# Optimization experiments

Measured on AMD Instinct MI355X. Metric: run time of the kernel, lower is better.

The kernel has to match this reference:

```python
import jax, jax.numpy as jnp
import numpy as np

TEMP = 0.07
N, D = 8192, 256
NUM_CLASSES = 512


def setup_inputs() -> dict:
    key = jax.random.key(0)
    k1, k2 = jax.random.split(key)
    features = jax.random.normal(k1, (N, D), dtype=jnp.float32)
    labels = jax.random.randint(k2, (N,), 0, NUM_CLASSES, dtype=jnp.int64)
    return {"features": features, "labels": labels}


def reference(features, labels):
    n = features.shape[0]
    # L2 normalize rows (torch F.normalize, eps=1e-12)
    norm = jnp.sqrt(jnp.sum(features * features, axis=1, keepdims=True))
    f = features / jnp.maximum(norm, 1e-12)
    # [N, N] cosine similarities scaled by temperature
    logits = jnp.matmul(f, f.T) / TEMP
    # positive-pair mask (same label), excluding self
    mask = (labels[:, None] == labels[None, :]).astype(logits.dtype)
    logits_mask = 1.0 - jnp.eye(n, dtype=logits.dtype)
    mask = mask * logits_mask
    # denominator excludes self-similarity
    exp_logits = jnp.exp(logits) * logits_mask
    log_prob = logits - jnp.log(jnp.sum(exp_logits, axis=1, keepdims=True) + 1e-6)
    mean_log_prob_pos = jnp.sum(mask * log_prob, axis=1) / jnp.clip(jnp.sum(mask, axis=1), 1.0, None)
    return -jnp.mean(mean_log_prob_pos)
```

## Files before the change

### kernel.cpp

```cpp
#include <hip/hip_runtime.h>
#include <hip/hip_bf16.h>

#define N 8192
#define D 256
#define NCLS 512
#define INV_TEMP 14.285714285714286f
#define C1 20.609929155f
#define JSPLIT 16

typedef __bf16 bf16x8 __attribute__((ext_vector_type(8)));
typedef float f32x4 __attribute__((ext_vector_type(4)));

static __device__ __forceinline__ unsigned short f2bf(float x) {
    unsigned int u = __float_as_uint(x);
    u = (u + 0x7fffu + ((u >> 16) & 1u)) >> 16;
    return (unsigned short)u;
}
static __device__ __forceinline__ float bf2f(unsigned short b) {
    return __uint_as_float(((unsigned int)b) << 16);
}

__global__ __launch_bounds__(256) void norm_kernel(const float* __restrict__ feat,
                                                   const int* __restrict__ labels,
                                                   __bf16* __restrict__ fb,
                                                   float* __restrict__ G) {
    const int row = (blockIdx.x * 256 + (int)threadIdx.x) >> 6;
    const int lane = threadIdx.x & 63;
    if (row >= N) return;
    float4 v = reinterpret_cast<const float4*>(feat + (size_t)row * D)[lane];
    float ss = v.x * v.x + v.y * v.y + v.z * v.z + v.w * v.w;
#pragma unroll
    for (int m = 1; m < 64; m <<= 1) ss += __shfl_xor(ss, m);
    const float inv = 1.0f / fmaxf(sqrtf(ss), 1e-12f);
    ushort4 o;
    o.x = f2bf(v.x * inv); o.y = f2bf(v.y * inv);
    o.z = f2bf(v.z * inv); o.w = f2bf(v.w * inv);
    reinterpret_cast<ushort4*>(fb + (size_t)row * D)[lane] = o;
    float* g = G + (size_t)labels[row] * D + lane * 4;
    atomicAdd(&g[0], bf2f(o.x));
    atomicAdd(&g[1], bf2f(o.y));
    atomicAdd(&g[2], bf2f(o.z));
    atomicAdd(&g[3], bf2f(o.w));
}

__global__ __launch_bounds__(256, 4) void supcon_main(const __bf16* __restrict__ fb,
                                                      float* __restrict__ rowD) {
    __shared__ __align__(1024) char lds[32768];
    const int lane = threadIdx.x & 63;
    const int w = threadIdx.x >> 6;
    const int l4 = lane & 15;
    const int lh = lane >> 4;
    const int wrow = blockIdx.x * 128 + w * 32;
    const int jbase = blockIdx.y * (N / JSPLIT);
    const char* fbb = (const char*)fb;

    bf16x8 a[2][8];
#pragma unroll
    for (int mf = 0; mf < 2; ++mf)
#pragma unroll
        for (int k = 0; k < 8; ++k)
            a[mf][k] = *reinterpret_cast<const bf16x8*>(
                fbb + (size_t)(wrow + mf * 16 + l4) * 512 + k * 64 + lh * 16);

    const int s7 = l4 & 7;
    const int lhx = lh ^ (s7 & 3);
    const int b2v = (s7 >> 2) & 1;
    const int rb_common = l4 * 512 + lhx * 16;

    auto stage = [&](int bufsel, int jb) {
#pragma unroll
        for (int r = 0; r < 4; ++r) {
            const int G = r * 256 + (int)threadIdx.x;
            const int row = G >> 5, h = G & 31;
            const char* src = fbb + (size_t)(jb + row) * 512 + ((h ^ (row & 7)) * 16);
            char* dst = lds + bufsel * 16384 + r * 4096 + w * 1024;
            __builtin_amdgcn_global_load_lds(
                (const __attribute__((address_space(1))) void*)src,
                (__attribute__((address_space(3))) void*)dst, 16, 0, 0);
        }
    };

    float dsum[2][4] = {};

    const int njt = (N / JSPLIT) / 32;
    int cur = 0;
    stage(0, jbase);
    __syncthreads();

    for (int jt = 0; jt < njt; ++jt) {
        const int jb = jbase + jt * 32;
        if (jt + 1 < njt) stage(cur ^ 1, jb + 32);

        const char* bb = lds + cur * 16384 + rb_common;
        const char* rb0 = bb + b2v * 64;
        const char* rb1 = bb + 64 - b2v * 64;

        f32x4 c[2][2] = {};
#pragma unroll
        for (int q = 0; q < 4; ++q) {
            bf16x8 b00 = *(const bf16x8*)(rb0 + q * 128);
            bf16x8 b01 = *(const bf16x8*)(rb0 + 8192 + q * 128);
            bf16x8 b10 = *(const bf16x8*)(rb1 + q * 128);
            bf16x8 b11 = *(const bf16x8*)(rb1 + 8192 + q * 128);
            c[0][0] = __builtin_amdgcn_mfma_f32_16x16x32_bf16(a[0][2 * q], b00, c[0][0], 0, 0, 0);
            c[1][0] = __builtin_amdgcn_mfma_f32_16x16x32_bf16(a[1][2 * q], b00, c[1][0], 0, 0, 0);
            c[0][1] = __builtin_amdgcn_mfma_f32_16x16x32_bf16(a[0][2 * q], b01, c[0][1], 0, 0, 0);
            c[1][1] = __builtin_amdgcn_mfma_f32_16x16x32_bf16(a[1][2 * q], b01, c[1][1], 0, 0, 0);
            c[0][0] = __builtin_amdgcn_mfma_f32_16x16x32_bf16(a[0][2 * q + 1], b10, c[0][0], 0, 0, 0);
            c[1][0] = __builtin_amdgcn_mfma_f32_16x16x32_bf16(a[1][2 * q + 1], b10, c[1][0], 0, 0, 0);
            c[0][1] = __builtin_amdgcn_mfma_f32_16x16x32_bf16(a[0][2 * q + 1], b11, c[0][1], 0, 0, 0);
            c[1][1] = __builtin_amdgcn_mfma_f32_16x16x32_bf16(a[1][2 * q + 1], b11, c[1][1], 0, 0, 0);
        }

#pragma unroll
        for (int mf = 0; mf < 2; ++mf) {
#pragma unroll
            for (int cf = 0; cf < 2; ++cf) {
                const f32x4 cc = c[mf][cf];
                if (wrow + mf * 16 == jb + cf * 16) {
#pragma unroll
                    for (int r = 0; r < 4; ++r) {
                        const bool diag = (l4 == lh * 4 + r);
                        dsum[mf][r] += diag ? 0.0f : __builtin_amdgcn_exp2f(cc[r] * C1);
                    }
                } else {
#pragma unroll
                    for (int r = 0; r < 4; ++r)
                        dsum[mf][r] += __builtin_amdgcn_exp2f(cc[r] * C1);
                }
            }
        }
        __syncthreads();
        cur ^= 1;
    }

#pragma unroll
    for (int mf = 0; mf < 2; ++mf) {
#pragma unroll
        for (int r = 0; r < 4; ++r) {
            float v1 = dsum[mf][r];
#pragma unroll
            for (int m = 1; m < 16; m <<= 1) v1 += __shfl_xor(v1, m);
            if (l4 == 0) atomicAdd(&rowD[wrow + mf * 16 + lh * 4 + r], v1);
        }
    }
}

__global__ __launch_bounds__(256) void rowdot_kernel(const __bf16* __restrict__ fb,
                                                     const int* __restrict__ labels,
                                                     const float* __restrict__ G,
                                                     float* __restrict__ rowS) {
    const int row = (blockIdx.x * 256 + (int)threadIdx.x) >> 6;
    const int lane = threadIdx.x & 63;
    if (row >= N) return;
    ushort4 o = reinterpret_cast<const ushort4*>(fb + (size_t)row * D)[lane];
    const float f0 = bf2f(o.x), f1 = bf2f(o.y), f2 = bf2f(o.z), f3 = bf2f(o.w);
    const float4 g = reinterpret_cast<const float4*>(G + (size_t)labels[row] * D)[lane];
    float dot = f0 * g.x + f1 * g.y + f2 * g.z + f3 * g.w;
    float self = f0 * f0 + f1 * f1 + f2 * f2 + f3 * f3;
#pragma unroll
    for (int m = 1; m < 64; m <<= 1) {
        dot += __shfl_xor(dot, m);
        self += __shfl_xor(self, m);
    }
    if (lane == 0) rowS[row] = (dot - self) * INV_TEMP;
}

__global__ __launch_bounds__(256) void finalize_kernel(const int* __restrict__ labels,
                                                       const float* __restrict__ rowD,
                                                       const float* __restrict__ rowS,
                                                       float* __restrict__ out) {
    __shared__ int hist[NCLS];
    __shared__ float red[4];
    for (int i = threadIdx.x; i < NCLS; i += 256) hist[i] = 0;
    __syncthreads();
    for (int i = threadIdx.x; i < N; i += 256) atomicAdd(&hist[labels[i]], 1);
    __syncthreads();
    float local = 0.0f;
    for (int r = threadIdx.x; r < N; r += 256) {
        const float c = (float)(hist[labels[r]] - 1);
        local += (rowS[r] - c * __logf(rowD[r] + 1e-6f)) / fmaxf(c, 1.0f);
    }
#pragma unroll
    for (int m = 1; m < 64; m <<= 1) local += __shfl_xor(local, m);
    if ((threadIdx.x & 63) == 0) red[threadIdx.x >> 6] = local;
    __syncthreads();
    if (threadIdx.x == 0) out[0] = -(red[0] + red[1] + red[2] + red[3]) / (float)N;
}

extern "C" void kernel_launch(void* const* d_in, const int* in_sizes, int n_in,
                              void* d_out, int out_size, void* d_ws, size_t ws_size,
                              hipStream_t stream) {
    const float* feat = (const float*)d_in[0];
    const int* labels = (const int*)d_in[1];

    __bf16* fb = (__bf16*)d_ws;
    float* G = (float*)((char*)d_ws + (size_t)N * D * 2);
    float* rowD = G + (size_t)NCLS * D;
    float* rowS = rowD + N;

    hipMemsetAsync(G, 0, ((size_t)NCLS * D + N) * sizeof(float), stream);
    norm_kernel<<<N / 4, 256, 0, stream>>>(feat, labels, fb, G);
    dim3 grid(N / 128, JSPLIT);
    supcon_main<<<grid, 256, 0, stream>>>(fb, rowD);
    rowdot_kernel<<<N / 4, 256, 0, stream>>>(fb, labels, G, rowS);
    finalize_kernel<<<1, 256, 0, stream>>>(labels, rowD, rowS, (float*)d_out);
}
```

Measured before the change: 143.8 us.

## Enlarge per-wave row tile and replace atomic class sums with ballot gather

The main GEMM kernel now gives each wave 64 rows (4 MFMA row fragments) instead of 32, so each B tile loaded from LDS is reused across twice as many rows. The grid halves in x and occupancy is lowered to 2 blocks per CU to fit the extra registers. Per-class feature sums are moved out of the norm kernel's float atomics into a separate kernel that uses ballots to gather member rows for two classes per block. The memset is dropped: rowD is zeroed in the norm kernel and G is fully overwritten. The trade-off is higher register pressure and lower occupancy against more MFMA reuse and no atomic contention, plus one extra kernel launch.

```diff
diff --git a/kernel.cpp b/kernel.cpp
--- a/kernel.cpp
+++ b/kernel.cpp
@@ -21,10 +21,11 @@
 }
 
 __global__ __launch_bounds__(256) void norm_kernel(const float* __restrict__ feat,
-                                                   const int* __restrict__ labels,
                                                    __bf16* __restrict__ fb,
-                                                   float* __restrict__ G) {
-    const int row = (blockIdx.x * 256 + (int)threadIdx.x) >> 6;
+                                                   float* __restrict__ rowD) {
+    const int gt = blockIdx.x * 256 + (int)threadIdx.x;
+    if (gt < N) rowD[gt] = 0.0f;
+    const int row = gt >> 6;
     const int lane = threadIdx.x & 63;
     if (row >= N) return;
     float4 v = reinterpret_cast<const float4*>(feat + (size_t)row * D)[lane];
@@ -36,27 +37,62 @@
     o.x = f2bf(v.x * inv); o.y = f2bf(v.y * inv);
     o.z = f2bf(v.z * inv); o.w = f2bf(v.w * inv);
     reinterpret_cast<ushort4*>(fb + (size_t)row * D)[lane] = o;
-    float* g = G + (size_t)labels[row] * D + lane * 4;
-    atomicAdd(&g[0], bf2f(o.x));
-    atomicAdd(&g[1], bf2f(o.y));
-    atomicAdd(&g[2], bf2f(o.z));
-    atomicAdd(&g[3], bf2f(o.w));
-}
-
-__global__ __launch_bounds__(256, 4) void supcon_main(const __bf16* __restrict__ fb,
+}
+
+__global__ __launch_bounds__(256) void classsum_kernel(const __bf16* __restrict__ fb,
+                                                       const int* __restrict__ labels,
+                                                       float* __restrict__ G) {
+    const int lane = threadIdx.x & 63;
+    const int w = threadIdx.x >> 6;
+    const int c0 = blockIdx.x * 2, c1 = c0 + 1;
+    float4 a0 = {0, 0, 0, 0}, a1 = {0, 0, 0, 0};
+    const int rbase = w * (N / 4);
+    for (int chunk = 0; chunk < N / 4; chunk += 64) {
+        const int lab = labels[rbase + chunk + lane];
+        unsigned long long m0 = __ballot(lab == c0);
+        unsigned long long m1 = __ballot(lab == c1);
+        while (m0) {
+            const int r = rbase + chunk + __builtin_ctzll(m0);
+            m0 &= m0 - 1;
+            ushort4 o = reinterpret_cast<const ushort4*>(fb + (size_t)r * D)[lane];
+            a0.x += bf2f(o.x); a0.y += bf2f(o.y); a0.z += bf2f(o.z); a0.w += bf2f(o.w);
+        }
+        while (m1) {
+            const int r = rbase + chunk + __builtin_ctzll(m1);
+            m1 &= m1 - 1;
+            ushort4 o = reinterpret_cast<const ushort4*>(fb + (size_t)r * D)[lane];
+            a1.x += bf2f(o.x); a1.y += bf2f(o.y); a1.z += bf2f(o.z); a1.w += bf2f(o.w);
+        }
+    }
+    __shared__ float4 part[4][2][64];
+    part[w][0][lane] = a0;
+    part[w][1][lane] = a1;
+    __syncthreads();
+    if (w < 2) {
+        float4 s = part[0][w][lane];
+        const float4 p1 = part[1][w][lane], p2 = part[2][w][lane], p3 = part[3][w][lane];
+        s.x += p1.x + p2.x + p3.x;
+        s.y += p1.y + p2.y + p3.y;
+        s.z += p1.z + p2.z + p3.z;
+        s.w += p1.w + p2.w + p3.w;
+        reinterpret_cast<float4*>(G + (size_t)(c0 + w) * D)[lane] = s;
+    }
+}
+
+__global__ __launch_bounds__(256, 2) void supcon_main(const __bf16* __restrict__ fb,
                                                       float* __restrict__ rowD) {
     __shared__ __align__(1024) char lds[32768];
     const int lane = threadIdx.x & 63;
     const int w = threadIdx.x >> 6;
     const int l4 = lane & 15;
     const int lh = lane >> 4;
-    const int wrow = blockIdx.x * 128 + w * 32;
+    const int wrow = blockIdx.x * 256 + w * 64;
     const int jbase = blockIdx.y * (N / JSPLIT);
     const char* fbb = (const char*)fb;
 
-    bf16x8 a[2][8];
-#pragma unroll
-    for (int mf = 0; mf < 2; ++mf)
+    bf16x8 a[4][8];
+#pragma unroll
+    for (int mf = 0; mf < 4; ++mf)
 #pragma unroll
         for (int k = 0; k < 8; ++k)
             a[mf][k] = *reinterpret_cast<const bf16x8*>(
@@ -70,8 +106,8 @@
     auto stage = [&](int bufsel, int jb) {
 #pragma unroll
         for (int r = 0; r < 4; ++r) {
-            const int G = r * 256 + (int)threadIdx.x;
-            const int row = G >> 5, h = G & 31;
+            const int gidx = r * 256 + (int)threadIdx.x;
+            const int row = gidx >> 5, h = gidx & 31;
             const char* src = fbb + (size_t)(jb + row) * 512 + ((h ^ (row & 7)) * 16);
             char* dst = lds + bufsel * 16384 + r * 4096 + w * 1024;
             __builtin_amdgcn_global_load_lds(
@@ -80,7 +116,7 @@
         }
     };
 
-    float dsum[2][4] = {};
+    float dsum[4][4] = {};
 
     const int njt = (N / JSPLIT) / 32;
     int cur = 0;
@@ -95,25 +131,24 @@
         const char* rb0 = bb + b2v * 64;
         const char* rb1 = bb + 64 - b2v * 64;
 
-        f32x4 c[2][2] = {};
+        f32x4 c[4][2] = {};
 #pragma unroll
         for (int q = 0; q < 4; ++q) {
             bf16x8 b00 = *(const bf16x8*)(rb0 + q * 128);
             bf16x8 b01 = *(const bf16x8*)(rb0 + 8192 + q * 128);
             bf16x8 b10 = *(const bf16x8*)(rb1 + q * 128);
             bf16x8 b11 = *(const bf16x8*)(rb1 + 8192 + q * 128);
-            c[0][0] = __builtin_amdgcn_mfma_f32_16x16x32_bf16(a[0][2 * q], b00, c[0][0], 0, 0, 0);
-            c[1][0] = __builtin_amdgcn_mfma_f32_16x16x32_bf16(a[1][2 * q], b00, c[1][0], 0, 0, 0);
-            c[0][1] = __builtin_amdgcn_mfma_f32_16x16x32_bf16(a[0][2 * q], b01, c[0][1], 0, 0, 0);
-            c[1][1] = __builtin_amdgcn_mfma_f32_16x16x32_bf16(a[1][2 * q], b01, c[1][1], 0, 0, 0);
-            c[0][0] = __builtin_amdgcn_mfma_f32_16x16x32_bf16(a[0][2 * q + 1], b10, c[0][0], 0, 0, 0);
-            c[1][0] = __builtin_amdgcn_mfma_f32_16x16x32_bf16(a[1][2 * q + 1], b10, c[1][0], 0, 0, 0);
-            c[0][1] = __builtin_amdgcn_mfma_f32_16x16x32_bf16(a[0][2 * q + 1], b11, c[0][1], 0, 0, 0);
-            c[1][1] = __builtin_amdgcn_mfma_f32_16x16x32_bf16(a[1][2 * q + 1], b11, c[1][1], 0, 0, 0);
-        }
-
-#pragma unroll
-        for (int mf = 0; mf < 2; ++mf) {
+#pragma unroll
+            for (int mf = 0; mf < 4; ++mf) {
+                c[mf][0] = __builtin_amdgcn_mfma_f32_16x16x32_bf16(a[mf][2 * q], b00, c[mf][0], 0, 0, 0);
+                c[mf][1] = __builtin_amdgcn_mfma_f32_16x16x32_bf16(a[mf][2 * q], b01, c[mf][1], 0, 0, 0);
+                c[mf][0] = __builtin_amdgcn_mfma_f32_16x16x32_bf16(a[mf][2 * q + 1], b10, c[mf][0], 0, 0, 0);
+                c[mf][1] = __builtin_amdgcn_mfma_f32_16x16x32_bf16(a[mf][2 * q + 1], b11, c[mf][1], 0, 0, 0);
+            }
+        }
+
+#pragma unroll
+        for (int mf = 0; mf < 4; ++mf) {
 #pragma unroll
             for (int cf = 0; cf < 2; ++cf) {
                 const f32x4 cc = c[mf][cf];
@@ -135,7 +170,7 @@
     }
 
 #pragma unroll
-    for (int mf = 0; mf < 2; ++mf) {
+    for (int mf = 0; mf < 4; ++mf) {
 #pragma unroll
         for (int r = 0; r < 4; ++r) {
             float v1 = dsum[mf][r];
@@ -199,9 +234,9 @@
     float* rowD = G + (size_t)NCLS * D;
     float* rowS = rowD + N;
 
-    hipMemsetAsync(G, 0, ((size_t)NCLS * D + N) * sizeof(float), stream);
-    norm_kernel<<<N / 4, 256, 0, stream>>>(feat, labels, fb, G);
-    dim3 grid(N / 128, JSPLIT);
+    norm_kernel<<<N / 4, 256, 0, stream>>>(feat, fb, rowD);
+    classsum_kernel<<<NCLS / 2, 256, 0, stream>>>(fb, labels, G);
+    dim3 grid(N / 256, JSPLIT);
     supcon_main<<<grid, 256, 0, stream>>>(fb, rowD);
     rowdot_kernel<<<N / 4, 256, 0, stream>>>(fb, labels, G, rowS);
     finalize_kernel<<<1, 256, 0, stream>>>(labels, rowD, rowS, (float*)d_out);
```

Result: faster. 126.7 us (-11.9%).
